# Optimization experiments

Measured on AMD Instinct MI355X. Metric: run time of the kernel, lower is better.

## Reference

```python
import jax, jax.numpy as jnp
import numpy as np

E, H, F = 1024, 16, 4096
WH, WW = 32, 32
B = 4
L = WH * WW           # 1024 cross-attn kv tokens
N = L + 1             # 1025 decoder tokens (CLS + window)
D = E // H
SCALE = D ** -0.5
NEG = -1e9            # stands in for -inf in the causal mask


def _rel_coords(Wh, Ww):
    coords = np.stack(np.meshgrid(np.arange(Wh), np.arange(Ww), indexing='ij')).reshape(2, -1)
    rc = (coords[:, :, None] - coords[:, None, :]).transpose(1, 2, 0).astype(np.int64)
    rc[:, :, 0] += Wh - 1
    rc[:, :, 1] += Ww - 1
    rc[:, :, 0] *= 2 * Ww - 1
    return rc.sum(-1)  # (L, L)


def rel_index_self(Wh, Ww):
    nrd = (2 * Wh - 1) * (2 * Ww - 1) + 3
    l = Wh * Ww
    idx = np.zeros((l + 1, l + 1), dtype=np.int32)
    idx[1:, 1:] = _rel_coords(Wh, Ww)
    idx[0, :] = nrd - 3
    idx[:, 0] = nrd - 2
    idx[0, 0] = nrd - 1
    return idx


def rel_index_cross(Wh, Ww):
    nrd = (2 * Wh - 1) * (2 * Ww - 1) + 1
    l = Wh * Ww
    idx = np.zeros((l + 1, l), dtype=np.int32)
    idx[1:, :] = _rel_coords(Wh, Ww)
    idx[0, :] = nrd - 1
    return idx


IDX_SELF = jnp.asarray(rel_index_self(WH, WW))    # (N, N) int32
IDX_CROSS = jnp.asarray(rel_index_cross(WH, WW))  # (N, L) int32
CAUSAL = jnp.triu(jnp.full((N, N), NEG, jnp.float32), 1)


def _ln(x, g, b, eps=1e-5):
    m = x.mean(-1, keepdims=True)
    v = ((x - m) ** 2).mean(-1, keepdims=True)
    return (x - m) * jax.lax.rsqrt(v + eps) * g + b


def setup_inputs():
    key = jax.random.key(0)
    ks = jax.random.split(key, 24)
    g = lambda i, shape, s=0.02: jax.random.normal(ks[i], shape, jnp.float32) * s
    return dict(
        x=g(0, (B, N, E), 1.0),
        y=g(1, (B, L, E), 1.0),
        norm1_g=jnp.ones((E,), jnp.float32), norm1_b=jnp.zeros((E,), jnp.float32),
        norm2_g=jnp.ones((E,), jnp.float32), norm2_b=jnp.zeros((E,), jnp.float32),
        norm3_g=jnp.ones((E,), jnp.float32), norm3_b=jnp.zeros((E,), jnp.float32),
        sa_qkv_w=g(2, (3 * E, E)),
        sa_q_bias=g(3, (E,)),
        sa_v_bias=g(4, (E,)),
        sa_rpb=g(5, ((2 * WH - 1) * (2 * WW - 1) + 3, H)),
        sa_proj_w=g(6, (E, E)), sa_proj_b=g(7, (E,)),
        ca_q_w=g(8, (E, E)),
        ca_kv_w=g(9, (2 * E, E)),
        ca_q_bias=g(10, (E,)),
        ca_v_bias=g(11, (E,)),
        ca_rpb=g(12, ((2 * WH - 1) * (2 * WW - 1) + 1, H)),
        ca_proj_w=g(13, (E, E)), ca_proj_b=g(14, (E,)),
        fc1_w=g(15, (F, E)), fc1_b=g(16, (F,)),
        fc2_w=g(17, (E, F)), fc2_b=g(18, (E,)),
        gamma1=jnp.full((E,), 0.1, jnp.float32),
        gamma2=jnp.full((E,), 0.1, jnp.float32),
        gamma3=jnp.full((E,), 0.1, jnp.float32),
    )


def reference(x, y, norm1_g, norm1_b, norm2_g, norm2_b, norm3_g, norm3_b,
              sa_qkv_w, sa_q_bias, sa_v_bias, sa_rpb, sa_proj_w, sa_proj_b,
              ca_q_w, ca_kv_w, ca_q_bias, ca_v_bias, ca_rpb, ca_proj_w, ca_proj_b,
              fc1_w, fc1_b, fc2_w, fc2_b, gamma1, gamma2, gamma3):
    # cross_attn.extract_kv(y): k gets zero bias, v gets v_bias
    kv_bias = jnp.concatenate([jnp.zeros((E,), x.dtype), ca_v_bias])
    kv = (y @ ca_kv_w.T + kv_bias).reshape(B, L, 2, H, D)
    ck = kv[:, :, 0].transpose(0, 2, 1, 3)  # (B,H,L,D)
    cv = kv[:, :, 1].transpose(0, 2, 1, 3)

    # --- causal self-attention with gathered relative-position bias ---
    h = _ln(x, norm1_g, norm1_b)
    qkv_bias = jnp.concatenate([sa_q_bias, jnp.zeros((E,), x.dtype), sa_v_bias])
    qkv = (h @ sa_qkv_w.T + qkv_bias).reshape(B, N, 3, H, D)
    q = qkv[:, :, 0].transpose(0, 2, 1, 3) * SCALE  # (B,H,N,D)
    k = qkv[:, :, 1].transpose(0, 2, 1, 3)
    v = qkv[:, :, 2].transpose(0, 2, 1, 3)
    bias = sa_rpb[IDX_SELF].transpose(2, 0, 1) + CAUSAL  # (H,N,N)
    attn = jnp.einsum('bhqd,bhkd->bhqk', q, k) + bias[None]
    attn = jax.nn.softmax(attn, axis=-1)
    sa = jnp.einsum('bhqk,bhkd->bhqd', attn, v).transpose(0, 2, 1, 3).reshape(B, N, E)
    sa = sa @ sa_proj_w.T + sa_proj_b
    x = x + gamma1 * sa

    # --- cross-attention with gathered relative-position bias ---
    h = _ln(x, norm2_g, norm2_b)
    q = (h @ ca_q_w.T + ca_q_bias).reshape(B, N, H, D).transpose(0, 2, 1, 3) * SCALE
    cbias = ca_rpb[IDX_CROSS].transpose(2, 0, 1)  # (H,N,L)
    attn = jnp.einsum('bhqd,bhkd->bhqk', q, ck) + cbias[None]
    attn = jax.nn.softmax(attn, axis=-1)
    ca = jnp.einsum('bhqk,bhkd->bhqd', attn, cv).transpose(0, 2, 1, 3).reshape(B, N, E)
    ca = ca @ ca_proj_w.T + ca_proj_b
    x = x + gamma2 * ca

    # --- FFN (Linear -> GELU -> Linear, no inner identity) ---
    h = _ln(x, norm3_g, norm3_b)
    h = jax.nn.gelu(h @ fc1_w.T + fc1_b, approximate=False)
    h = h @ fc2_w.T + fc2_b
    x = x + gamma3 * h
    return x
```

## Files before the change

kernel.cpp:

```cpp
#include <hip/hip_runtime.h>
#include <hip/hip_bf16.h>
#include <math.h>

typedef __bf16 bf16;
typedef __bf16 bf16x8 __attribute__((ext_vector_type(8)));
typedef float f32x4 __attribute__((ext_vector_type(4)));

#define MP    4224
#define MACT  4100
#define NQTOK 1025
#define NKTOK 1024
#define EDIM  1024
#define FDIM  4096
#define NHEAD 16
#define HD    64
#define QSCALE 0.125f
#define VTS   1056
#define NROWS 65600

__device__ __forceinline__ void glds16(const bf16* g, bf16* l) {
  __builtin_amdgcn_global_load_lds(
      (const __attribute__((address_space(1))) void*)g,
      (__attribute__((address_space(3))) void*)l, 16, 0, 0);
}

__device__ __forceinline__ bf16x8 ld8(const void* p, size_t i, bool f32) {
  if (f32) {
    const float* q = (const float*)p + i;
    bf16x8 r;
#pragma unroll
    for (int j = 0; j < 8; ++j) r[j] = (bf16)q[j];
    return r;
  }
  return *(const bf16x8*)((const bf16*)p + i);
}

struct WPtrs { const float* s[8]; };
__global__ __launch_bounds__(256) void conv_kernel(WPtrs wp, bf16* dst) {
  const size_t sz[8] = {3145728UL, 1048576UL, 1048576UL, 2097152UL,
                        1048576UL, 4194304UL, 4194304UL, 4194304UL};
  size_t id = ((size_t)blockIdx.x * 256 + threadIdx.x) * 8;
  size_t off = 0;
#pragma unroll
  for (int i = 0; i < 8; ++i) {
    if (id < off + sz[i]) {
      const float* s = wp.s[i] + (id - off);
      bf16x8 r;
#pragma unroll
      for (int j = 0; j < 8; ++j) r[j] = (bf16)s[j];
      *(bf16x8*)(dst + id) = r;
      return;
    }
    off += sz[i];
  }
}

__global__ void zero_pads_kernel(bf16* hln) {
  int i = blockIdx.x * 256 + threadIdx.x;
  const int n = (MP - MACT) * EDIM;
  if (i < n) hln[(size_t)MACT * EDIM + i] = (bf16)0.0f;
}

template<bool FIRST>
__global__ __launch_bounds__(256) void ln_kernel(const float* __restrict__ src,
    float* __restrict__ xf, bf16* __restrict__ out,
    const float* __restrict__ g, const float* __restrict__ bta) {
  const int row = blockIdx.x;
  const int tid = threadIdx.x;
  float v[4];
#pragma unroll
  for (int i = 0; i < 4; ++i) {
    v[i] = src[(size_t)row * EDIM + tid + i * 256];
    if (FIRST) xf[(size_t)row * EDIM + tid + i * 256] = v[i];
  }
  float s = 0.f, sq = 0.f;
#pragma unroll
  for (int i = 0; i < 4; ++i) { s += v[i]; sq += v[i] * v[i]; }
#pragma unroll
  for (int m = 32; m >= 1; m >>= 1) {
    s += __shfl_xor(s, m);
    sq += __shfl_xor(sq, m);
  }
  __shared__ float ss[4], ssq[4];
  const int wave = tid >> 6;
  if ((tid & 63) == 0) { ss[wave] = s; ssq[wave] = sq; }
  __syncthreads();
  s = ss[0] + ss[1] + ss[2] + ss[3];
  sq = ssq[0] + ssq[1] + ssq[2] + ssq[3];
  const float mean = s * (1.f / EDIM);
  const float var = sq * (1.f / EDIM) - mean * mean;
  const float rstd = rsqrtf(var + 1e-5f);
#pragma unroll
  for (int i = 0; i < 4; ++i) {
    int e = tid + i * 256;
    out[(size_t)row * EDIM + e] = (bf16)((v[i] - mean) * rstd * g[e] + bta[e]);
  }
}

__global__ __launch_bounds__(256) void fc2_reduce_kernel(
    const float* __restrict__ p0, const float* __restrict__ xf,
    const float* __restrict__ bias, const float* __restrict__ gamma,
    float* __restrict__ outf) {
  size_t i = ((size_t)blockIdx.x * 256 + threadIdx.x) * 4;
  if (i >= (size_t)MACT * EDIM) return;
  f32x4 a = *(const f32x4*)(p0 + i);
  f32x4 b = *(const f32x4*)(outf + i);
  f32x4 x = *(const f32x4*)(xf + i);
  const int gn = (int)(i & (EDIM - 1));
  f32x4 r;
#pragma unroll
  for (int j = 0; j < 4; ++j)
    r[j] = x[j] + gamma[gn + j] * (a[j] + b[j] + bias[gn + j]);
  *(f32x4*)(outf + i) = r;
}

__global__ __launch_bounds__(256) void attn_combine_kernel(
    const bf16* __restrict__ opart, const float* __restrict__ mlbuf,
    bf16* __restrict__ out) {
  const int tid = threadIdx.x;
  const int row = blockIdx.x * 32 + (tid >> 3);
  const int d0 = (tid & 7) * 8;
  if (row >= NROWS) return;
  const float m0 = mlbuf[(size_t)row * 2],           l0 = mlbuf[(size_t)row * 2 + 1];
  const float m1 = mlbuf[((size_t)NROWS + row) * 2], l1 = mlbuf[((size_t)NROWS + row) * 2 + 1];
  const float M = fmaxf(m0, m1);
  float w0 = __expf(m0 - M) * l0;
  float w1 = __expf(m1 - M) * l1;
  const float den = w0 + w1;
  const float sc = (den > 0.f) ? 1.f / den : 0.f;
  w0 *= sc; w1 *= sc;
  const size_t OPSZ = (size_t)NROWS * HD;
  bf16x8 a = *(const bf16x8*)(opart + (size_t)row * HD + d0);
  bf16x8 c = *(const bf16x8*)(opart + OPSZ + (size_t)row * HD + d0);
  const int b = row / (NHEAD * NQTOK);
  const int rem = row - b * (NHEAD * NQTOK);
  const int h = rem / NQTOK;
  const int q = rem - h * NQTOK;
  bf16x8 o;
#pragma unroll
  for (int j = 0; j < 8; ++j)
    o[j] = (bf16)(w0 * (float)a[j] + w1 * (float)c[j]);
  *(bf16x8*)(out + ((size_t)b * NQTOK + q) * EDIM + h * HD + d0) = o;
}

enum { EPI_QKV = 0, EPI_KV = 1, EPI_Q = 2, EPI_RES = 3, EPI_GELU = 4,
       EPI_FINAL = 5, EPI_PART = 6 };

template<int EPI, bool ASY>
__global__ __launch_bounds__(256) void gemm_bt(
    const void* __restrict__ A, const void* __restrict__ Bw,
    int K, int Kc,
    const float* __restrict__ bias0, const float* __restrict__ bias1,
    const float* __restrict__ gamma, float* __restrict__ xf,
    bf16* __restrict__ out0, bf16* __restrict__ out1, bf16* __restrict__ out2,
    float* __restrict__ outf)
{
  constexpr int LDP = ASY ? 32 : 40;
  __shared__ bf16 As[2][128][LDP];
  __shared__ bf16 Bs[2][128][LDP];
  const int tid = threadIdx.x;
  const int lane = tid & 63, wave = tid >> 6;
  const int quad = lane >> 4, l16 = lane & 15;
  const int wr = wave >> 1, wc = wave & 1;
  const int m0 = blockIdx.y * 128, n0 = blockIdx.x * 128;
  const int kbase = blockIdx.z * Kc;
  const bool first = (blockIdx.z == 0);
  const int r0 = tid >> 2, c0 = (tid & 3) * 8;

  const bf16* gA = nullptr; const bf16* gB = nullptr;
  if (ASY) {
    gA = (const bf16*)A + (size_t)(m0 + wave * 16 + (lane >> 2)) * K + kbase + (lane & 3) * 8;
    gB = (const bf16*)Bw + (size_t)(n0 + wave * 16 + (lane >> 2)) * K + kbase + (lane & 3) * 8;
  }

  auto stage = [&](int bi, int kk) {
    if (ASY) {
      const bf16* pA = gA + kk;
      const bf16* pB = gB + kk;
      bf16* la = &As[bi][wave * 16][0];
      bf16* lb = &Bs[bi][wave * 16][0];
      glds16(pA, la);
      glds16(pA + (size_t)64 * K, la + 64 * LDP);
      glds16(pB, lb);
      glds16(pB + (size_t)64 * K, lb + 64 * LDP);
    } else {
      const bool f32a = (EPI == EPI_KV);
      const size_t kkk = (size_t)(kbase + kk);
      *(bf16x8*)(&As[bi][r0][c0])      = ld8(A,  (size_t)(m0 + r0) * K + kkk + c0, f32a);
      *(bf16x8*)(&As[bi][r0 + 64][c0]) = ld8(A,  (size_t)(m0 + r0 + 64) * K + kkk + c0, f32a);
      *(bf16x8*)(&Bs[bi][r0][c0])      = ld8(Bw, (size_t)(n0 + r0) * K + kkk + c0, true);
      *(bf16x8*)(&Bs[bi][r0 + 64][c0]) = ld8(Bw, (size_t)(n0 + r0 + 64) * K + kkk + c0, true);
    }
  };

  f32x4 acc[4][4];
#pragma unroll
  for (int i = 0; i < 4; ++i)
#pragma unroll
    for (int j = 0; j < 4; ++j)
#pragma unroll
      for (int r = 0; r < 4; ++r) acc[i][j][r] = 0.f;

  stage(0, 0);
  __syncthreads();
  int buf = 0;
  for (int k0 = 0; k0 < Kc; k0 += 32) {
    if (k0 + 32 < Kc) stage(buf ^ 1, k0 + 32);
    bf16x8 af[4], bfv[4];
#pragma unroll
    for (int i = 0; i < 4; ++i) {
      af[i]  = *(const bf16x8*)(&As[buf][wr * 64 + i * 16 + l16][quad * 8]);
      bfv[i] = *(const bf16x8*)(&Bs[buf][wc * 64 + i * 16 + l16][quad * 8]);
    }
#pragma unroll
    for (int mb = 0; mb < 4; ++mb)
#pragma unroll
      for (int nb = 0; nb < 4; ++nb)
        acc[mb][nb] = __builtin_amdgcn_mfma_f32_16x16x32_bf16(af[mb], bfv[nb], acc[mb][nb], 0, 0, 0);
    __syncthreads();
    buf ^= 1;
  }

#pragma unroll
  for (int mb = 0; mb < 4; ++mb) {
#pragma unroll
    for (int r = 0; r < 4; ++r) {
      const int gm = m0 + wr * 64 + mb * 16 + quad * 4 + r;
#pragma unroll
      for (int nb = 0; nb < 4; ++nb) {
        const int gn = n0 + wc * 64 + nb * 16 + l16;
        float v = acc[mb][nb][r];
        if (EPI == EPI_QKV) {
          if (gm < MACT) {
            unsigned b = (unsigned)gm / 1025u;
            unsigned t = (unsigned)gm - b * 1025u;
            int sec = gn >> 10, e = gn & 1023;
            int h = e >> 6, d = e & 63;
            if (sec == 0)
              out0[((size_t)(b * NHEAD + h) * NQTOK + t) * HD + d] =
                  (bf16)((v + bias0[e]) * QSCALE);
            else if (sec == 1)
              out1[((size_t)(b * NHEAD + h) * NQTOK + t) * HD + d] = (bf16)v;
            else
              out2[((size_t)(b * NHEAD + h) * HD + d) * VTS + t] =
                  (bf16)(v + bias1[e]);
          }
        } else if (EPI == EPI_KV) {
          unsigned b = (unsigned)gm >> 10;
          unsigned t = (unsigned)gm & 1023u;
          int sec = gn >> 10, e = gn & 1023;
          int h = e >> 6, d = e & 63;
          if (sec == 0)
            out0[((size_t)(b * NHEAD + h) * NKTOK + t) * HD + d] = (bf16)v;
          else
            out1[((size_t)(b * NHEAD + h) * HD + d) * NKTOK + t] =
                (bf16)(v + bias1[e]);
        } else if (EPI == EPI_Q) {
          if (gm < MACT) {
            unsigned b = (unsigned)gm / 1025u;
            unsigned t = (unsigned)gm - b * 1025u;
            int h = gn >> 6, d = gn & 63;
            out0[((size_t)(b * NHEAD + h) * NQTOK + t) * HD + d] =
                (bf16)((v + bias0[gn]) * QSCALE);
          }
        } else if (EPI == EPI_RES) {
          if (gm < MACT) {
            size_t o = (size_t)gm * EDIM + gn;
            xf[o] += gamma[gn] * (v + bias0[gn]);
          }
        } else if (EPI == EPI_GELU) {
          float z = v + bias0[gn];
          float ge = 0.5f * z * (1.0f + erff(z * 0.70710678118f));
          out0[(size_t)gm * FDIM + gn] = (bf16)ge;
        } else if (EPI == EPI_PART) {
          if (gm < MACT) {
            float* dst = first ? xf : outf;
            dst[(size_t)gm * EDIM + gn] = v;
          }
        } else {
          if (gm < MACT) {
            size_t o = (size_t)gm * EDIM + gn;
            float add = gamma[gn] * (v + (first ? bias0[gn] : 0.f));
            if (first) add += xf[o];
            atomicAdd(&outf[o], add);
          }
        }
      }
    }
  }
}

template<bool CROSS>
__global__ __launch_bounds__(256) void attn_kernel(
    const bf16* __restrict__ Qg, const bf16* __restrict__ Kg,
    const bf16* __restrict__ Vg, const float* __restrict__ rpb,
    bf16* __restrict__ opart, float* __restrict__ mlbuf)
{
  const int NK  = CROSS ? NKTOK : NQTOK;
  const int NRD = CROSS ? 3970 : 3972;
  const int VS  = CROSS ? NKTOK : VTS;
  const int qt  = CROSS ? blockIdx.x : (16 - blockIdx.x);
  const int h = blockIdx.y;
  const int b = blockIdx.z & 3, s = blockIdx.z >> 2;
  const int tid = threadIdx.x;
  const int lane = tid & 63, wave = tid >> 6;
  const int quad = lane >> 4, l16 = lane & 15;

  __shared__ bf16 rpb_s[4096];
  __shared__ bf16 Ks[64][72];
  __shared__ bf16 Vt[64][72];

  for (int i = tid; i < 4096; i += 256)
    rpb_s[i] = (bf16)((i < NRD) ? rpb[(size_t)i * NHEAD + h] : 0.f);

  const int q0 = qt * 64;
  const int qrow = q0 + wave * 16 + l16;
  const size_t qhb = (size_t)(b * NHEAD + h) * NQTOK;
  bf16x8 qf0, qf1;
  if (qrow < NQTOK) {
    qf0 = *(const bf16x8*)(Qg + (qhb + qrow) * HD + quad * 8);
    qf1 = *(const bf16x8*)(Qg + (qhb + qrow) * HD + 32 + quad * 8);
  } else {
#pragma unroll
    for (int j = 0; j < 8; ++j) { qf0[j] = (bf16)0.f; qf1[j] = (bf16)0.f; }
  }

  const int qg = qrow;
  const int qp = qg - 1;
  const int qcode = (qg > 0) ? ((qp >> 5) * 63 + (qp & 31) + 1984) : 0;

  int ib[4][4];
#pragma unroll
  for (int kb = 0; kb < 4; ++kb)
#pragma unroll
    for (int r = 0; r < 4; ++r) {
      const int o = kb * 16 + quad * 4 + r;
      const int om = CROSS ? o : (o - 1);
      const int ocode = (om >> 5) * 63 + (om & 31);
      ib[kb][r] = qcode - ocode;
    }
  const bool q0cls = (q0 == 0);

  float m_run = -1e30f, l_run = 0.f;
  f32x4 oacc[4];
#pragma unroll
  for (int d = 0; d < 4; ++d)
#pragma unroll
    for (int r = 0; r < 4; ++r) oacc[d][r] = 0.f;

  const size_t kvbK = (size_t)(b * NHEAD + h) * NK;
  const size_t vbase = (size_t)(b * NHEAD + h) * HD;
  const int nch = CROSS ? (NKTOK / 64) : (qt + 1);

  const int rr = tid >> 3;
  const int co = (tid & 7) * 8;

  const int srcA = (quad & 1) * 32 + l16;
  const int srcB = srcA + 16;

  bf16x8 krg[2], vrg[2];
  auto stage_load = [&](int c) {
    const int kc = c * 64;
#pragma unroll
    for (int vv = 0; vv < 2; ++vv) {
      const int row = rr + vv * 32;
      if (!CROSS && kc + row >= NK) {
#pragma unroll
        for (int j = 0; j < 8; ++j) krg[vv][j] = (bf16)0.f;
      } else {
        krg[vv] = *(const bf16x8*)(Kg + (kvbK + kc + row) * HD + co);
      }
      if (!CROSS && kc + co >= NK) {
#pragma unroll
        for (int j = 0; j < 8; ++j) vrg[vv][j] = (bf16)0.f;
      } else {
        vrg[vv] = *(const bf16x8*)(Vg + (vbase + row) * VS + kc + co);
      }
    }
  };

  if (s < nch) stage_load(s);
  int c126 = s * 126;
  for (int c = s; c < nch; c += 2) {
    const int kc = c * 64;
    if (c != s) __syncthreads();
#pragma unroll
    for (int vv = 0; vv < 2; ++vv) {
      const int row = rr + vv * 32;
      *(bf16x8*)(&Ks[row][co]) = krg[vv];
      *(bf16x8*)(&Vt[row][co]) = vrg[vv];
    }
    __syncthreads();
    if (c + 2 < nch) stage_load(c + 2);

    f32x4 aacc[4];
    __builtin_amdgcn_s_setprio(1);
#pragma unroll
    for (int kb = 0; kb < 4; ++kb) {
      bf16x8 kf0 = *(const bf16x8*)(&Ks[kb * 16 + l16][quad * 8]);
      bf16x8 kf1 = *(const bf16x8*)(&Ks[kb * 16 + l16][32 + quad * 8]);
      f32x4 a;
#pragma unroll
      for (int r = 0; r < 4; ++r) a[r] = 0.f;
      a = __builtin_amdgcn_mfma_f32_16x16x32_bf16(kf0, qf0, a, 0, 0, 0);
      a = __builtin_amdgcn_mfma_f32_16x16x32_bf16(kf1, qf1, a, 0, 0, 0);
      aacc[kb] = a;
    }
    __builtin_amdgcn_s_setprio(0);

    float sv[4][4];
    const bool lastc = (!CROSS) && (c == nch - 1);
    const bool firstc = (c == 0);
    if (!lastc) {
#pragma unroll
      for (int kb = 0; kb < 4; ++kb)
#pragma unroll
        for (int r = 0; r < 4; ++r) {
          int idx = ib[kb][r] - c126;
          if (q0cls) { if (qg == 0) idx = 3969; }
          if (!CROSS && firstc && kb == 0 && r == 0) {
            if (quad == 0) idx = (qg == 0) ? 3971 : 3970;
          }
          idx &= 4095;
          sv[kb][r] = aacc[kb][r] + (float)rpb_s[idx];
        }
    } else {
#pragma unroll
      for (int kb = 0; kb < 4; ++kb)
#pragma unroll
        for (int r = 0; r < 4; ++r) {
          int idx = ib[kb][r] - c126;
          if (q0cls) { if (qg == 0) idx = 3969; }
          if (firstc && kb == 0 && r == 0) {
            if (quad == 0) idx = (qg == 0) ? 3971 : 3970;
          }
          idx &= 4095;
          const int kg = kc + kb * 16 + quad * 4 + r;
          const bool valid = (kg < NK) && (kg <= qg);
          sv[kb][r] = valid ? (aacc[kb][r] + (float)rpb_s[idx]) : -1e30f;
        }
    }
    c126 += 252;

    float mx = sv[0][0];
#pragma unroll
    for (int kb = 0; kb < 4; ++kb)
#pragma unroll
      for (int r = 0; r < 4; ++r) mx = fmaxf(mx, sv[kb][r]);
    mx = fmaxf(mx, __shfl_xor(mx, 16));
    mx = fmaxf(mx, __shfl_xor(mx, 32));

    if (!__all(mx - m_run <= 8.f)) {
      const float mnew = fmaxf(m_run, mx);
      const float alpha = __expf(m_run - mnew);
      m_run = mnew;
      l_run *= alpha;
      float alr[4];
#pragma unroll
      for (int r = 0; r < 4; ++r) alr[r] = __shfl(alpha, quad * 4 + r);
#pragma unroll
      for (int d = 0; d < 4; ++d)
#pragma unroll
        for (int r = 0; r < 4; ++r) oacc[d][r] *= alr[r];
    }

    float rs = 0.f;
    unsigned pk[4][2];
#pragma unroll
    for (int kb = 0; kb < 4; ++kb) {
      float p0 = __expf(sv[kb][0] - m_run);
      float p1 = __expf(sv[kb][1] - m_run);
      float p2 = __expf(sv[kb][2] - m_run);
      float p3 = __expf(sv[kb][3] - m_run);
      rs += (p0 + p1) + (p2 + p3);
      union { __bf16 h[2]; unsigned u; } w0, w1;
      w0.h[0] = (bf16)p0; w0.h[1] = (bf16)p1;
      w1.h[0] = (bf16)p2; w1.h[1] = (bf16)p3;
      pk[kb][0] = w0.u; pk[kb][1] = w1.u;
    }
    rs += __shfl_xor(rs, 16);
    rs += __shfl_xor(rs, 32);
    l_run += rs;

    union { unsigned u[4]; bf16x8 v; } f0, f1;
#pragma unroll
    for (int p = 0; p < 4; ++p) {
      const int src = (p < 2) ? srcA : srcB;
      unsigned a0 = (unsigned)__shfl((int)pk[0][p & 1], src);
      unsigned a1 = (unsigned)__shfl((int)pk[1][p & 1], src);
      unsigned b0 = (unsigned)__shfl((int)pk[2][p & 1], src);
      unsigned b1 = (unsigned)__shfl((int)pk[3][p & 1], src);
      f0.u[p] = (quad < 2) ? a0 : a1;
      f1.u[p] = (quad < 2) ? b0 : b1;
    }

    __builtin_amdgcn_s_setprio(1);
#pragma unroll
    for (int db = 0; db < 4; ++db) {
      bf16x8 vf0 = *(const bf16x8*)(&Vt[db * 16 + l16][quad * 8]);
      bf16x8 vf1 = *(const bf16x8*)(&Vt[db * 16 + l16][32 + quad * 8]);
      oacc[db] = __builtin_amdgcn_mfma_f32_16x16x32_bf16(f0.v, vf0, oacc[db], 0, 0, 0);
      oacc[db] = __builtin_amdgcn_mfma_f32_16x16x32_bf16(f1.v, vf1, oacc[db], 0, 0, 0);
    }
    __builtin_amdgcn_s_setprio(0);
  }

  const size_t OPSZ = (size_t)NROWS * HD;
#pragma unroll
  for (int r = 0; r < 4; ++r) {
    const int qo = q0 + wave * 16 + quad * 4 + r;
    if (qo < NQTOK) {
      const float lr = __shfl(l_run, quad * 4 + r);
      const float inv = (lr > 0.f) ? 1.f / lr : 0.f;
      const size_t orow = (size_t)(b * NHEAD + h) * NQTOK + qo;
#pragma unroll
      for (int db = 0; db < 4; ++db)
        opart[(size_t)s * OPSZ + orow * HD + db * 16 + l16] =
            (bf16)(oacc[db][r] * inv);
    }
  }
  if (quad == 0 && qrow < NQTOK) {
    const size_t orow = (size_t)(b * NHEAD + h) * NQTOK + qrow;
    mlbuf[((size_t)s * NROWS + orow) * 2 + 0] = m_run;
    mlbuf[((size_t)s * NROWS + orow) * 2 + 1] = l_run;
  }
}

extern "C" void kernel_launch(void* const* d_in, const int* in_sizes, int n_in,
                              void* d_out, int out_size, void* d_ws, size_t ws_size,
                              hipStream_t stream) {
  (void)in_sizes; (void)n_in; (void)out_size;
  const float* x        = (const float*)d_in[0];
  const float* y        = (const float*)d_in[1];
  const float* n1g      = (const float*)d_in[2];
  const float* n1b      = (const float*)d_in[3];
  const float* n2g      = (const float*)d_in[4];
  const float* n2b      = (const float*)d_in[5];
  const float* n3g      = (const float*)d_in[6];
  const float* n3b      = (const float*)d_in[7];
  const float* sa_qkv_w = (const float*)d_in[8];
  const float* sa_qb    = (const float*)d_in[9];
  const float* sa_vb    = (const float*)d_in[10];
  const float* sa_rpb   = (const float*)d_in[11];
  const float* sa_pw    = (const float*)d_in[12];
  const float* sa_pb    = (const float*)d_in[13];
  const float* ca_qw    = (const float*)d_in[14];
  const float* ca_kvw   = (const float*)d_in[15];
  const float* ca_qb    = (const float*)d_in[16];
  const float* ca_vb    = (const float*)d_in[17];
  const float* ca_rpb   = (const float*)d_in[18];
  const float* ca_pw    = (const float*)d_in[19];
  const float* ca_pb    = (const float*)d_in[20];
  const float* fc1_w    = (const float*)d_in[21];
  const float* fc1_b    = (const float*)d_in[22];
  const float* fc2_w    = (const float*)d_in[23];
  const float* fc2_b    = (const float*)d_in[24];
  const float* g1       = (const float*)d_in[25];
  const float* g2       = (const float*)d_in[26];
  const float* g3       = (const float*)d_in[27];
  float* outf = (float*)d_out;
  bf16* opart = (bf16*)d_out;

  char* w = (char*)d_ws;
  float* xf = (float*)w;  w += (size_t)MP * EDIM * 4;
  bf16* hln = (bf16*)w;   w += (size_t)MP * EDIM * 2;
  char* big = w;          w += (size_t)MP * FDIM * 2;
  const size_t qkv_sz = (size_t)4 * NHEAD * NQTOK * HD * 2;
  bf16* qt = (bf16*)big;
  bf16* kt = (bf16*)(big + qkv_sz);
  bf16* vt = (bf16*)(big + 2 * qkv_sz);
  bf16* h1 = (bf16*)big;
  float* mlf = (float*)(big + 26214400UL);
  bf16* wpool = (bf16*)w; w += 20971520UL * 2;
  const bool asy = ((size_t)(w - (char*)d_ws) <= ws_size);

  bf16* qkvw_b = wpool;
  bf16* pw_b   = qkvw_b + 3145728UL;
  bf16* cqw_b  = pw_b   + 1048576UL;
  bf16* ckvw_b = cqw_b  + 1048576UL;
  bf16* cpw_b  = ckvw_b + 2097152UL;
  bf16* fc1w_b = cpw_b  + 1048576UL;
  bf16* fc2w_b = fc1w_b + 4194304UL;
  bf16* y_b    = fc2w_b + 4194304UL;
  float* part0 = (float*)wpool;

  if (asy) {
    WPtrs wp = {{sa_qkv_w, sa_pw, ca_qw, ca_kvw, ca_pw, fc1_w, fc2_w, y}};
    conv_kernel<<<10240, 256, 0, stream>>>(wp, wpool);
  }
  zero_pads_kernel<<<dim3(((MP - MACT) * EDIM + 255) / 256), 256, 0, stream>>>(hln);

  ln_kernel<true><<<MACT, 256, 0, stream>>>(x, xf, hln, n1g, n1b);
  if (asy) gemm_bt<EPI_QKV, true><<<dim3(24, 33, 1), 256, 0, stream>>>(hln, qkvw_b, 1024, 1024,
      sa_qb, sa_vb, nullptr, nullptr, qt, kt, vt, nullptr);
  else     gemm_bt<EPI_QKV, false><<<dim3(24, 33, 1), 256, 0, stream>>>(hln, sa_qkv_w, 1024, 1024,
      sa_qb, sa_vb, nullptr, nullptr, qt, kt, vt, nullptr);
  attn_kernel<false><<<dim3(17, NHEAD, 8), 256, 0, stream>>>(qt, kt, vt, sa_rpb, opart, mlf);
  attn_combine_kernel<<<dim3(NROWS / 32), 256, 0, stream>>>(opart, mlf, hln);
  if (asy) gemm_bt<EPI_RES, true><<<dim3(8, 33, 1), 256, 0, stream>>>(hln, pw_b, 1024, 1024,
      sa_pb, nullptr, g1, xf, nullptr, nullptr, nullptr, nullptr);
  else     gemm_bt<EPI_RES, false><<<dim3(8, 33, 1), 256, 0, stream>>>(hln, sa_pw, 1024, 1024,
      sa_pb, nullptr, g1, xf, nullptr, nullptr, nullptr, nullptr);

  ln_kernel<false><<<MACT, 256, 0, stream>>>(xf, nullptr, hln, n2g, n2b);
  if (asy) gemm_bt<EPI_Q, true><<<dim3(8, 33, 1), 256, 0, stream>>>(hln, cqw_b, 1024, 1024,
      ca_qb, nullptr, nullptr, nullptr, qt, nullptr, nullptr, nullptr);
  else     gemm_bt<EPI_Q, false><<<dim3(8, 33, 1), 256, 0, stream>>>(hln, ca_qw, 1024, 1024,
      ca_qb, nullptr, nullptr, nullptr, qt, nullptr, nullptr, nullptr);
  if (asy) gemm_bt<EPI_KV, true><<<dim3(16, 32, 1), 256, 0, stream>>>(y_b, ckvw_b, 1024, 1024,
      nullptr, ca_vb, nullptr, nullptr, kt, vt, nullptr, nullptr);
  else     gemm_bt<EPI_KV, false><<<dim3(16, 32, 1), 256, 0, stream>>>(y, ca_kvw, 1024, 1024,
      nullptr, ca_vb, nullptr, nullptr, kt, vt, nullptr, nullptr);
  attn_kernel<true><<<dim3(17, NHEAD, 8), 256, 0, stream>>>(qt, kt, vt, ca_rpb, opart, mlf);
  attn_combine_kernel<<<dim3(NROWS / 32), 256, 0, stream>>>(opart, mlf, hln);
  if (asy) gemm_bt<EPI_RES, true><<<dim3(8, 33, 1), 256, 0, stream>>>(hln, cpw_b, 1024, 1024,
      ca_pb, nullptr, g2, xf, nullptr, nullptr, nullptr, nullptr);
  else     gemm_bt<EPI_RES, false><<<dim3(8, 33, 1), 256, 0, stream>>>(hln, ca_pw, 1024, 1024,
      ca_pb, nullptr, g2, xf, nullptr, nullptr, nullptr, nullptr);

  ln_kernel<false><<<MACT, 256, 0, stream>>>(xf, nullptr, hln, n3g, n3b);
  if (asy) gemm_bt<EPI_GELU, true><<<dim3(32, 33, 1), 256, 0, stream>>>(hln, fc1w_b, 1024, 1024,
      fc1_b, nullptr, nullptr, nullptr, h1, nullptr, nullptr, nullptr);
  else     gemm_bt<EPI_GELU, false><<<dim3(32, 33, 1), 256, 0, stream>>>(hln, fc1_w, 1024, 1024,
      fc1_b, nullptr, nullptr, nullptr, h1, nullptr, nullptr, nullptr);
  if (asy) {
    gemm_bt<EPI_PART, true><<<dim3(8, 33, 2), 256, 0, stream>>>(h1, fc2w_b, 4096, 2048,
        nullptr, nullptr, nullptr, part0, nullptr, nullptr, nullptr, outf);
    fc2_reduce_kernel<<<dim3(4100), 256, 0, stream>>>(part0, xf, fc2_b, g3, outf);
  } else {
    hipMemsetAsync(outf, 0, (size_t)MACT * EDIM * 4, stream);
    gemm_bt<EPI_FINAL, false><<<dim3(8, 33, 4), 256, 0, stream>>>(h1, fc2_w, 4096, 1024,
        fc2_b, nullptr, g3, xf, nullptr, nullptr, nullptr, outf);
  }
}
```

Before: 675.2 us.

## Process two 16-row query tiles per wave in attention to reuse K/V tiles

The attention kernel now gives each wave two 16-query sub-tiles (128 queries per block), so every K and V tile loaded into shared memory serves twice as many MFMAs. The grid shrinks from 17 to 9 query blocks, and the causal chunk count and masking cover the last two chunks. It adds a launch-bounds occupancy hint. This cuts per-query LDS traffic and global K/V reloads, at the cost of doubled accumulator registers and fewer blocks.

```diff
diff --git a/kernel.cpp b/kernel.cpp
--- a/kernel.cpp
+++ b/kernel.cpp
@@ -291,7 +291,7 @@
 }
 
 template<bool CROSS>
-__global__ __launch_bounds__(256) void attn_kernel(
+__global__ __launch_bounds__(256, 4) void attn_kernel(
     const bf16* __restrict__ Qg, const bf16* __restrict__ Kg,
     const bf16* __restrict__ Vg, const float* __restrict__ rpb,
     bf16* __restrict__ opart, float* __restrict__ mlbuf)
@@ -299,7 +299,7 @@
   const int NK  = CROSS ? NKTOK : NQTOK;
   const int NRD = CROSS ? 3970 : 3972;
   const int VS  = CROSS ? NKTOK : VTS;
-  const int qt  = CROSS ? blockIdx.x : (16 - blockIdx.x);
+  const int qt  = CROSS ? blockIdx.x : (8 - blockIdx.x);
   const int h = blockIdx.y;
   const int b = blockIdx.z & 3, s = blockIdx.z >> 2;
   const int tid = threadIdx.x;
@@ -313,21 +313,31 @@
   for (int i = tid; i < 4096; i += 256)
     rpb_s[i] = (bf16)((i < NRD) ? rpb[(size_t)i * NHEAD + h] : 0.f);
 
-  const int q0 = qt * 64;
-  const int qrow = q0 + wave * 16 + l16;
+  const int q0 = qt * 128;
+  const int qA = q0 + wave * 32 + l16;
+  const int qB = qA + 16;
   const size_t qhb = (size_t)(b * NHEAD + h) * NQTOK;
-  bf16x8 qf0, qf1;
-  if (qrow < NQTOK) {
-    qf0 = *(const bf16x8*)(Qg + (qhb + qrow) * HD + quad * 8);
-    qf1 = *(const bf16x8*)(Qg + (qhb + qrow) * HD + 32 + quad * 8);
+  bf16x8 qfA0, qfA1, qfB0, qfB1;
+  if (qA < NQTOK) {
+    qfA0 = *(const bf16x8*)(Qg + (qhb + qA) * HD + quad * 8);
+    qfA1 = *(const bf16x8*)(Qg + (qhb + qA) * HD + 32 + quad * 8);
   } else {
 #pragma unroll
-    for (int j = 0; j < 8; ++j) { qf0[j] = (bf16)0.f; qf1[j] = (bf16)0.f; }
-  }
-
-  const int qg = qrow;
-  const int qp = qg - 1;
-  const int qcode = (qg > 0) ? ((qp >> 5) * 63 + (qp & 31) + 1984) : 0;
+    for (int j = 0; j < 8; ++j) { qfA0[j] = (bf16)0.f; qfA1[j] = (bf16)0.f; }
+  }
+  if (qB < NQTOK) {
+    qfB0 = *(const bf16x8*)(Qg + (qhb + qB) * HD + quad * 8);
+    qfB1 = *(const bf16x8*)(Qg + (qhb + qB) * HD + 32 + quad * 8);
+  } else {
+#pragma unroll
+    for (int j = 0; j < 8; ++j) { qfB0[j] = (bf16)0.f; qfB1[j] = (bf16)0.f; }
+  }
+
+  const int qpA = qA - 1;
+  const int qcodeA = (qA > 0) ? ((qpA >> 5) * 63 + (qpA & 31) + 1984) : 0;
+  const int qpB = qB - 1;
+  const int qcodeB = ((qpB >> 5) * 63 + (qpB & 31) + 1984);
+  const int dq = qcodeB - qcodeA;
 
   int ib[4][4];
 #pragma unroll
@@ -337,20 +347,20 @@
       const int o = kb * 16 + quad * 4 + r;
       const int om = CROSS ? o : (o - 1);
       const int ocode = (om >> 5) * 63 + (om & 31);
-      ib[kb][r] = qcode - ocode;
-    }
-  const bool q0cls = (q0 == 0);
-
-  float m_run = -1e30f, l_run = 0.f;
-  f32x4 oacc[4];
+      ib[kb][r] = qcodeA - ocode;
+    }
+  const bool waveCls = (q0 == 0 && wave == 0);
+
+  float mA = -1e30f, lA = 0.f, mB = -1e30f, lB = 0.f;
+  f32x4 oaccA[4], oaccB[4];
 #pragma unroll
   for (int d = 0; d < 4; ++d)
 #pragma unroll
-    for (int r = 0; r < 4; ++r) oacc[d][r] = 0.f;
+    for (int r = 0; r < 4; ++r) { oaccA[d][r] = 0.f; oaccB[d][r] = 0.f; }
 
   const size_t kvbK = (size_t)(b * NHEAD + h) * NK;
   const size_t vbase = (size_t)(b * NHEAD + h) * HD;
-  const int nch = CROSS ? (NKTOK / 64) : (qt + 1);
+  const int nch = CROSS ? (NKTOK / 64) : min(2 * qt + 2, 17);
 
   const int rr = tid >> 3;
   const int co = (tid & 7) * 8;
@@ -393,105 +403,142 @@
     __syncthreads();
     if (c + 2 < nch) stage_load(c + 2);
 
-    f32x4 aacc[4];
-    __builtin_amdgcn_s_setprio(1);
+    float svA[4][4], svB[4][4];
+    const bool maskc = (!CROSS) && (c >= nch - 2);
+    const bool firstc = (c == 0);
 #pragma unroll
     for (int kb = 0; kb < 4; ++kb) {
       bf16x8 kf0 = *(const bf16x8*)(&Ks[kb * 16 + l16][quad * 8]);
       bf16x8 kf1 = *(const bf16x8*)(&Ks[kb * 16 + l16][32 + quad * 8]);
-      f32x4 a;
-#pragma unroll
-      for (int r = 0; r < 4; ++r) a[r] = 0.f;
-      a = __builtin_amdgcn_mfma_f32_16x16x32_bf16(kf0, qf0, a, 0, 0, 0);
-      a = __builtin_amdgcn_mfma_f32_16x16x32_bf16(kf1, qf1, a, 0, 0, 0);
-      aacc[kb] = a;
-    }
-    __builtin_amdgcn_s_setprio(0);
-
-    float sv[4][4];
-    const bool lastc = (!CROSS) && (c == nch - 1);
-    const bool firstc = (c == 0);
-    if (!lastc) {
+      f32x4 a, bb;
+#pragma unroll
+      for (int r = 0; r < 4; ++r) { a[r] = 0.f; bb[r] = 0.f; }
+      __builtin_amdgcn_s_setprio(1);
+      a  = __builtin_amdgcn_mfma_f32_16x16x32_bf16(kf0, qfA0, a, 0, 0, 0);
+      a  = __builtin_amdgcn_mfma_f32_16x16x32_bf16(kf1, qfA1, a, 0, 0, 0);
+      bb = __builtin_amdgcn_mfma_f32_16x16x32_bf16(kf0, qfB0, bb, 0, 0, 0);
+      bb = __builtin_amdgcn_mfma_f32_16x16x32_bf16(kf1, qfB1, bb, 0, 0, 0);
+      __builtin_amdgcn_s_setprio(0);
+#pragma unroll
+      for (int r = 0; r < 4; ++r) {
+        int idxA = ib[kb][r] - c126;
+        int idxB = idxA + dq;
+        if (waveCls) { if (qA == 0) idxA = 3969; }
+        if (!CROSS && firstc && kb == 0 && r == 0 && quad == 0) {
+          idxA = (qA == 0) ? 3971 : 3970;
+          idxB = 3970;
+        }
+        idxA &= 4095; idxB &= 4095;
+        if (!maskc) {
+          svA[kb][r] = a[r]  + (float)rpb_s[idxA];
+          svB[kb][r] = bb[r] + (float)rpb_s[idxB];
+        } else {
+          const int kg = kc + kb * 16 + quad * 4 + r;
+          const bool vA = (kg < NK) && (kg <= qA);
+          const bool vB = (kg < NK) && (kg <= qB);
+          svA[kb][r] = vA ? (a[r]  + (float)rpb_s[idxA]) : -1e30f;
+          svB[kb][r] = vB ? (bb[r] + (float)rpb_s[idxB]) : -1e30f;
+        }
+      }
+    }
+    c126 += 252;
+
+    union { unsigned u[4]; bf16x8 v; } fA0, fA1, fB0, fB1;
+    {
+      float mx = svA[0][0];
 #pragma unroll
       for (int kb = 0; kb < 4; ++kb)
 #pragma unroll
-        for (int r = 0; r < 4; ++r) {
-          int idx = ib[kb][r] - c126;
-          if (q0cls) { if (qg == 0) idx = 3969; }
-          if (!CROSS && firstc && kb == 0 && r == 0) {
-            if (quad == 0) idx = (qg == 0) ? 3971 : 3970;
-          }
-          idx &= 4095;
-          sv[kb][r] = aacc[kb][r] + (float)rpb_s[idx];
-        }
-    } else {
+        for (int r = 0; r < 4; ++r) mx = fmaxf(mx, svA[kb][r]);
+      mx = fmaxf(mx, __shfl_xor(mx, 16));
+      mx = fmaxf(mx, __shfl_xor(mx, 32));
+      if (!__all(mx - mA <= 8.f)) {
+        const float mnew = fmaxf(mA, mx);
+        const float alpha = __expf(mA - mnew);
+        mA = mnew; lA *= alpha;
+        float alr[4];
+#pragma unroll
+        for (int r = 0; r < 4; ++r) alr[r] = __shfl(alpha, quad * 4 + r);
+#pragma unroll
+        for (int d = 0; d < 4; ++d)
+#pragma unroll
+          for (int r = 0; r < 4; ++r) oaccA[d][r] *= alr[r];
+      }
+      float rs = 0.f;
+      unsigned pk[4][2];
+#pragma unroll
+      for (int kb = 0; kb < 4; ++kb) {
+        float p0 = __expf(svA[kb][0] - mA);
+        float p1 = __expf(svA[kb][1] - mA);
+        float p2 = __expf(svA[kb][2] - mA);
+        float p3 = __expf(svA[kb][3] - mA);
+        rs += (p0 + p1) + (p2 + p3);
+        union { __bf16 h[2]; unsigned u; } w0, w1;
+        w0.h[0] = (bf16)p0; w0.h[1] = (bf16)p1;
+        w1.h[0] = (bf16)p2; w1.h[1] = (bf16)p3;
+        pk[kb][0] = w0.u; pk[kb][1] = w1.u;
+      }
+      rs += __shfl_xor(rs, 16);
+      rs += __shfl_xor(rs, 32);
+      lA += rs;
+#pragma unroll
+      for (int p = 0; p < 4; ++p) {
+        const int src = (p < 2) ? srcA : srcB;
+        unsigned a0 = (unsigned)__shfl((int)pk[0][p & 1], src);
+        unsigned a1 = (unsigned)__shfl((int)pk[1][p & 1], src);
+        unsigned b0 = (unsigned)__shfl((int)pk[2][p & 1], src);
+        unsigned b1 = (unsigned)__shfl((int)pk[3][p & 1], src);
+        fA0.u[p] = (quad < 2) ? a0 : a1;
+        fA1.u[p] = (quad < 2) ? b0 : b1;
+      }
+    }
+    {
+      float mx = svB[0][0];
 #pragma unroll
       for (int kb = 0; kb < 4; ++kb)
 #pragma unroll
-        for (int r = 0; r < 4; ++r) {
-          int idx = ib[kb][r] - c126;
-          if (q0cls) { if (qg == 0) idx = 3969; }
-          if (firstc && kb == 0 && r == 0) {
-            if (quad == 0) idx = (qg == 0) ? 3971 : 3970;
-          }
-          idx &= 4095;
-          const int kg = kc + kb * 16 + quad * 4 + r;
-          const bool valid = (kg < NK) && (kg <= qg);
-          sv[kb][r] = valid ? (aacc[kb][r] + (float)rpb_s[idx]) : -1e30f;
-        }
-    }
-    c126 += 252;
-
-    float mx = sv[0][0];
-#pragma unroll
-    for (int kb = 0; kb < 4; ++kb)
-#pragma unroll
-      for (int r = 0; r < 4; ++r) mx = fmaxf(mx, sv[kb][r]);
-    mx = fmaxf(mx, __shfl_xor(mx, 16));
-    mx = fmaxf(mx, __shfl_xor(mx, 32));
-
-    if (!__all(mx - m_run <= 8.f)) {
-      const float mnew = fmaxf(m_run, mx);
-      const float alpha = __expf(m_run - mnew);
-      m_run = mnew;
-      l_run *= alpha;
-      float alr[4];
-#pragma unroll
-      for (int r = 0; r < 4; ++r) alr[r] = __shfl(alpha, quad * 4 + r);
-#pragma unroll
-      for (int d = 0; d < 4; ++d)
-#pragma unroll
-        for (int r = 0; r < 4; ++r) oacc[d][r] *= alr[r];
-    }
-
-    float rs = 0.f;
-    unsigned pk[4][2];
-#pragma unroll
-    for (int kb = 0; kb < 4; ++kb) {
-      float p0 = __expf(sv[kb][0] - m_run);
-      float p1 = __expf(sv[kb][1] - m_run);
-      float p2 = __expf(sv[kb][2] - m_run);
-      float p3 = __expf(sv[kb][3] - m_run);
-      rs += (p0 + p1) + (p2 + p3);
-      union { __bf16 h[2]; unsigned u; } w0, w1;
-      w0.h[0] = (bf16)p0; w0.h[1] = (bf16)p1;
-      w1.h[0] = (bf16)p2; w1.h[1] = (bf16)p3;
-      pk[kb][0] = w0.u; pk[kb][1] = w1.u;
-    }
-    rs += __shfl_xor(rs, 16);
-    rs += __shfl_xor(rs, 32);
-    l_run += rs;
-
-    union { unsigned u[4]; bf16x8 v; } f0, f1;
-#pragma unroll
-    for (int p = 0; p < 4; ++p) {
-      const int src = (p < 2) ? srcA : srcB;
-      unsigned a0 = (unsigned)__shfl((int)pk[0][p & 1], src);
-      unsigned a1 = (unsigned)__shfl((int)pk[1][p & 1], src);
-      unsigned b0 = (unsigned)__shfl((int)pk[2][p & 1], src);
-      unsigned b1 = (unsigned)__shfl((int)pk[3][p & 1], src);
-      f0.u[p] = (quad < 2) ? a0 : a1;
-      f1.u[p] = (quad < 2) ? b0 : b1;
+        for (int r = 0; r < 4; ++r) mx = fmaxf(mx, svB[kb][r]);
+      mx = fmaxf(mx, __shfl_xor(mx, 16));
+      mx = fmaxf(mx, __shfl_xor(mx, 32));
+      if (!__all(mx - mB <= 8.f)) {
+        const float mnew = fmaxf(mB, mx);
+        const float alpha = __expf(mB - mnew);
+        mB = mnew; lB *= alpha;
+        float alr[4];
+#pragma unroll
+        for (int r = 0; r < 4; ++r) alr[r] = __shfl(alpha, quad * 4 + r);
+#pragma unroll
+        for (int d = 0; d < 4; ++d)
+#pragma unroll
+          for (int r = 0; r < 4; ++r) oaccB[d][r] *= alr[r];
+      }
+      float rs = 0.f;
+      unsigned pk[4][2];
+#pragma unroll
+      for (int kb = 0; kb < 4; ++kb) {
+        float p0 = __expf(svB[kb][0] - mB);
+        float p1 = __expf(svB[kb][1] - mB);
+        float p2 = __expf(svB[kb][2] - mB);
+        float p3 = __expf(svB[kb][3] - mB);
+        rs += (p0 + p1) + (p2 + p3);
+        union { __bf16 h[2]; unsigned u; } w0, w1;
+        w0.h[0] = (bf16)p0; w0.h[1] = (bf16)p1;
+        w1.h[0] = (bf16)p2; w1.h[1] = (bf16)p3;
+        pk[kb][0] = w0.u; pk[kb][1] = w1.u;
+      }
+      rs += __shfl_xor(rs, 16);
+      rs += __shfl_xor(rs, 32);
+      lB += rs;
+#pragma unroll
+      for (int p = 0; p < 4; ++p) {
+        const int src = (p < 2) ? srcA : srcB;
+        unsigned a0 = (unsigned)__shfl((int)pk[0][p & 1], src);
+        unsigned a1 = (unsigned)__shfl((int)pk[1][p & 1], src);
+        unsigned b0 = (unsigned)__shfl((int)pk[2][p & 1], src);
+        unsigned b1 = (unsigned)__shfl((int)pk[3][p & 1], src);
+        fB0.u[p] = (quad < 2) ? a0 : a1;
+        fB1.u[p] = (quad < 2) ? b0 : b1;
+      }
     }
 
     __builtin_amdgcn_s_setprio(1);
@@ -499,8 +546,10 @@
     for (int db = 0; db < 4; ++db) {
       bf16x8 vf0 = *(const bf16x8*)(&Vt[db * 16 + l16][quad * 8]);
       bf16x8 vf1 = *(const bf16x8*)(&Vt[db * 16 + l16][32 + quad * 8]);
-      oacc[db] = __builtin_amdgcn_mfma_f32_16x16x32_bf16(f0.v, vf0, oacc[db], 0, 0, 0);
-      oacc[db] = __builtin_amdgcn_mfma_f32_16x16x32_bf16(f1.v, vf1, oacc[db], 0, 0, 0);
+      oaccA[db] = __builtin_amdgcn_mfma_f32_16x16x32_bf16(fA0.v, vf0, oaccA[db], 0, 0, 0);
+      oaccA[db] = __builtin_amdgcn_mfma_f32_16x16x32_bf16(fA1.v, vf1, oaccA[db], 0, 0, 0);
+      oaccB[db] = __builtin_amdgcn_mfma_f32_16x16x32_bf16(fB0.v, vf0, oaccB[db], 0, 0, 0);
+      oaccB[db] = __builtin_amdgcn_mfma_f32_16x16x32_bf16(fB1.v, vf1, oaccB[db], 0, 0, 0);
     }
     __builtin_amdgcn_s_setprio(0);
   }
@@ -508,21 +557,38 @@
   const size_t OPSZ = (size_t)NROWS * HD;
 #pragma unroll
   for (int r = 0; r < 4; ++r) {
-    const int qo = q0 + wave * 16 + quad * 4 + r;
-    if (qo < NQTOK) {
-      const float lr = __shfl(l_run, quad * 4 + r);
+    const int qoA = q0 + wave * 32 + quad * 4 + r;
+    if (qoA < NQTOK) {
+      const float lr = __shfl(lA, quad * 4 + r);
       const float inv = (lr > 0.f) ? 1.f / lr : 0.f;
-      const size_t orow = (size_t)(b * NHEAD + h) * NQTOK + qo;
+      const size_t orow = (size_t)(b * NHEAD + h) * NQTOK + qoA;
 #pragma unroll
       for (int db = 0; db < 4; ++db)
         opart[(size_t)s * OPSZ + orow * HD + db * 16 + l16] =
-            (bf16)(oacc[db][r] * inv);
-    }
-  }
-  if (quad == 0 && qrow < NQTOK) {
-    const size_t orow = (size_t)(b * NHEAD + h) * NQTOK + qrow;
-    mlbuf[((size_t)s * NROWS + orow) * 2 + 0] = m_run;
-    mlbuf[((size_t)s * NROWS + orow) * 2 + 1] = l_run;
+            (bf16)(oaccA[db][r] * inv);
+    }
+    const int qoB = qoA + 16;
+    if (qoB < NQTOK) {
+      const float lr = __shfl(lB, quad * 4 + r);
+      const float inv = (lr > 0.f) ? 1.f / lr : 0.f;
+      const size_t orow = (size_t)(b * NHEAD + h) * NQTOK + qoB;
+#pragma unroll
+      for (int db = 0; db < 4; ++db)
+        opart[(size_t)s * OPSZ + orow * HD + db * 16 + l16] =
+            (bf16)(oaccB[db][r] * inv);
+    }
+  }
+  if (quad == 0) {
+    if (qA < NQTOK) {
+      const size_t orow = (size_t)(b * NHEAD + h) * NQTOK + qA;
+      mlbuf[((size_t)s * NROWS + orow) * 2 + 0] = mA;
+      mlbuf[((size_t)s * NROWS + orow) * 2 + 1] = lA;
+    }
+    if (qB < NQTOK) {
+      const size_t orow = (size_t)(b * NHEAD + h) * NQTOK + qB;
+      mlbuf[((size_t)s * NROWS + orow) * 2 + 0] = mB;
+      mlbuf[((size_t)s * NROWS + orow) * 2 + 1] = lB;
+    }
   }
 }
 
@@ -595,7 +661,7 @@
       sa_qb, sa_vb, nullptr, nullptr, qt, kt, vt, nullptr);
   else     gemm_bt<EPI_QKV, false><<<dim3(24, 33, 1), 256, 0, stream>>>(hln, sa_qkv_w, 1024, 1024,
       sa_qb, sa_vb, nullptr, nullptr, qt, kt, vt, nullptr);
-  attn_kernel<false><<<dim3(17, NHEAD, 8), 256, 0, stream>>>(qt, kt, vt, sa_rpb, opart, mlf);
+  attn_kernel<false><<<dim3(9, NHEAD, 8), 256, 0, stream>>>(qt, kt, vt, sa_rpb, opart, mlf);
   attn_combine_kernel<<<dim3(NROWS / 32), 256, 0, stream>>>(opart, mlf, hln);
   if (asy) gemm_bt<EPI_RES, true><<<dim3(8, 33, 1), 256, 0, stream>>>(hln, pw_b, 1024, 1024,
       sa_pb, nullptr, g1, xf, nullptr, nullptr, nullptr, nullptr);
@@ -611,7 +677,7 @@
       nullptr, ca_vb, nullptr, nullptr, kt, vt, nullptr, nullptr);
   else     gemm_bt<EPI_KV, false><<<dim3(16, 32, 1), 256, 0, stream>>>(y, ca_kvw, 1024, 1024,
       nullptr, ca_vb, nullptr, nullptr, kt, vt, nullptr, nullptr);
-  attn_kernel<true><<<dim3(17, NHEAD, 8), 256, 0, stream>>>(qt, kt, vt, ca_rpb, opart, mlf);
+  attn_kernel<true><<<dim3(9, NHEAD, 8), 256, 0, stream>>>(qt, kt, vt, ca_rpb, opart, mlf);
   attn_combine_kernel<<<dim3(NROWS / 32), 256, 0, stream>>>(opart, mlf, hln);
   if (asy) gemm_bt<EPI_RES, true><<<dim3(8, 33, 1), 256, 0, stream>>>(hln, cpw_b, 1024, 1024,
       ca_pb, nullptr, g2, xf, nullptr, nullptr, nullptr, nullptr);
```

Measured after the change: 853.0 us. 26.3% more time.
